# Optimization experiments

Measured on AMD Instinct MI355X. Metric: run time of the kernel, lower is better.

## Reference

```python
import jax, jax.numpy as jnp
import numpy as np

SCALING = 32.0 / 16  # alpha / rank


def setup_inputs() -> dict:
    key = jax.random.key(0)
    k1, k2, k3, k4, k5 = jax.random.split(key, 5)
    B, S, IN, OUT, R = 4, 2048, 4096, 4096, 16
    x = jax.random.normal(k1, (B, S, IN), dtype=jnp.float32)
    weight = jax.random.normal(k2, (OUT, IN), dtype=jnp.float32) * 0.02
    lora_a_w = jax.random.normal(k3, (R, IN), dtype=jnp.float32) * 0.02
    lora_b_w = jax.random.normal(k4, (OUT, R), dtype=jnp.float32) * 0.02
    magnitude = jax.random.uniform(k5, (OUT,), dtype=jnp.float32) + 0.5
    return {"x": x, "weight": weight, "lora_a_w": lora_a_w,
            "lora_b_w": lora_b_w, "magnitude": magnitude}


def reference(x, weight, lora_a_w, lora_b_w, magnitude):
    # base linear: x @ W^T  -> [..., out_dim]
    base_out = jnp.einsum('bsi,oi->bso', x, weight)
    # low-rank path (dropout is identity at p=0.0)
    lora_out = jnp.einsum('bsr,or->bso', jnp.einsum('bsi,ri->bsr', x, lora_a_w), lora_b_w)
    # merged low-rank weight B @ A (torch uses an eye-matrix trick; direct matmul is equivalent)
    lora_weight = lora_b_w @ lora_a_w  # [out, in]
    # row-wise norm of adapted weight; detached in the original
    weight_norm = jax.lax.stop_gradient(
        jnp.linalg.norm(weight + SCALING * lora_weight, axis=1))  # [out]
    mag_norm_scale = (magnitude / weight_norm)[None, None, :]  # [1,1,out]
    dora_out = (mag_norm_scale - 1.0) * base_out + mag_norm_scale * lora_out * SCALING
    return dora_out + base_out
```

## Files before the change

### kernel.cpp

```cpp
#include <hip/hip_runtime.h>
#include <hip/hip_bf16.h>
#include <stdint.h>

#define M_DIM 8192
#define N_DIM 4096
#define K_DIM 4096
#define R_DIM 16

#define PREP_BLOCKS 256
#define CAST_BLOCKS 8192

typedef __attribute__((ext_vector_type(8))) short bf16x8;
typedef __attribute__((ext_vector_type(4))) float f32x4;

__device__ __forceinline__ unsigned short f2bf(float f) {
  union { float f; unsigned int u; } v; v.f = f;
  unsigned int r = 0x7FFFu + ((v.u >> 16) & 1u);
  return (unsigned short)((v.u + r) >> 16);
}

__device__ __forceinline__ void gload16(const unsigned short* g, unsigned short* l) {
  __builtin_amdgcn_global_load_lds(
      (const __attribute__((address_space(1))) void*)g,
      (__attribute__((address_space(3))) void*)l,
      16, 0, 0);
}

__global__ void __launch_bounds__(256) prep_kernel(
    const float4* __restrict__ x4, ushort4* __restrict__ xbf4,
    const float* __restrict__ W, const float* __restrict__ Aw,
    const float* __restrict__ Bw, const float* __restrict__ mag,
    unsigned short* __restrict__ wbf, float* __restrict__ scale) {
  const int tid = threadIdx.x;

  if (blockIdx.x >= PREP_BLOCKS) {
    const int base = (blockIdx.x - PREP_BLOCKS) * 1024 + tid;
    #pragma unroll
    for (int u = 0; u < 4; ++u) {
      const int i = base + u * 256;
      float4 f = x4[i];
      ushort4 o;
      o.x = f2bf(f.x); o.y = f2bf(f.y); o.z = f2bf(f.z); o.w = f2bf(f.w);
      xbf4[i] = o;
    }
    return;
  }

  __shared__ float AwS[16 * 1024];
  __shared__ float BoS[16 * 16];
  __shared__ float red[16 * 4];
  const int o0 = blockIdx.x * 16;

  BoS[tid] = Bw[(o0 + (tid >> 4)) * R_DIM + (tid & 15)];

  float ss[16];
  #pragma unroll
  for (int i = 0; i < 16; ++i) ss[i] = 0.f;

  const float4* W4  = (const float4*)W;
  const float4* Aw4 = (const float4*)Aw;
  ushort4* wbf4 = (ushort4*)wbf;

  for (int c = 0; c < 4; ++c) {
    __syncthreads();
    #pragma unroll
    for (int t = tid; t < 4096; t += 256) {
      const int r  = t >> 8;
      const int j4 = t & 255;
      ((float4*)AwS)[r * 256 + j4] = Aw4[(size_t)r * 1024 + c * 256 + j4];
    }
    __syncthreads();
    #pragma unroll 4
    for (int i = 0; i < 16; ++i) {
      float4 w = W4[((size_t)(o0 + i) * K_DIM + c * 1024) / 4 + tid];
      float4 acc = {0.f, 0.f, 0.f, 0.f};
      #pragma unroll
      for (int r = 0; r < R_DIM; ++r) {
        const float b = BoS[i * 16 + r];
        const float4 a = ((const float4*)AwS)[r * 256 + tid];
        acc.x += b * a.x; acc.y += b * a.y; acc.z += b * a.z; acc.w += b * a.w;
      }
      float4 v;
      v.x = w.x + 2.f * acc.x; v.y = w.y + 2.f * acc.y;
      v.z = w.z + 2.f * acc.z; v.w = w.w + 2.f * acc.w;
      ss[i] += v.x * v.x + v.y * v.y + v.z * v.z + v.w * v.w;
      ushort4 o;
      o.x = f2bf(v.x); o.y = f2bf(v.y); o.z = f2bf(v.z); o.w = f2bf(v.w);
      wbf4[((size_t)(o0 + i) * K_DIM + c * 1024) / 4 + tid] = o;
    }
  }

  const int lane = tid & 63, wave = tid >> 6;
  #pragma unroll
  for (int i = 0; i < 16; ++i) {
    float s = ss[i];
    #pragma unroll
    for (int off = 32; off > 0; off >>= 1) s += __shfl_down(s, off, 64);
    if (lane == 0) red[i * 4 + wave] = s;
  }
  __syncthreads();
  if (tid < 16) {
    const float s = red[tid * 4] + red[tid * 4 + 1] + red[tid * 4 + 2] + red[tid * 4 + 3];
    scale[o0 + tid] = mag[o0 + tid] / sqrtf(s);
  }
}

__global__ void __launch_bounds__(256)
dora_gemm(const unsigned short* __restrict__ A,
          const unsigned short* __restrict__ Bt,
          const float* __restrict__ scale,
          float* __restrict__ C) {
  __shared__ __align__(16) unsigned short As[128 * 32];
  __shared__ __align__(16) unsigned short Bs[128 * 32];
  const int tid  = threadIdx.x;
  const int lane = tid & 63;
  const int wave = tid >> 6;
  const int bM = blockIdx.y * 128;
  const int bN = blockIdx.x * 128;

  const int sr = lane >> 2;
  const int sc = (((lane & 3) ^ ((lane >> 3) & 3)) * 8);
  const unsigned short* pa0 = A  + (size_t)(bM + wave * 32 + sr) * K_DIM + sc;
  const unsigned short* pa1 = pa0 + (size_t)16 * K_DIM;
  const unsigned short* pb0 = Bt + (size_t)(bN + wave * 32 + sr) * K_DIM + sc;
  const unsigned short* pb1 = pb0 + (size_t)16 * K_DIM;
  unsigned short* lA0 = &As[wave * 32 * 32];
  unsigned short* lA1 = lA0 + 16 * 32;
  unsigned short* lB0 = &Bs[wave * 32 * 32];
  unsigned short* lB1 = lB0 + 16 * 32;

  const int fr = lane & 15;
  const int fq = lane >> 4;
  const int xr = (fr >> 1) & 3;
  const int cA = (fq ^ xr) * 8;
  const int wM = (wave >> 1) * 64;
  const int wN = (wave & 1) * 64;

  f32x4 acc[4][4];
  #pragma unroll
  for (int i = 0; i < 4; ++i)
    #pragma unroll
    for (int j = 0; j < 4; ++j) acc[i][j] = (f32x4){0.f, 0.f, 0.f, 0.f};

  for (int k0 = 0; k0 < K_DIM; k0 += 32) {
    gload16(pa0 + k0, lA0);
    gload16(pa1 + k0, lA1);
    gload16(pb0 + k0, lB0);
    gload16(pb1 + k0, lB1);
    __syncthreads();
    bf16x8 aF[4], bF[4];
    #pragma unroll
    for (int mt = 0; mt < 4; ++mt)
      aF[mt] = *(const bf16x8*)&As[(wM + mt * 16 + fr) * 32 + cA];
    #pragma unroll
    for (int nt = 0; nt < 4; ++nt)
      bF[nt] = *(const bf16x8*)&Bs[(wN + nt * 16 + fr) * 32 + cA];
    #pragma unroll
    for (int mt = 0; mt < 4; ++mt)
      #pragma unroll
      for (int nt = 0; nt < 4; ++nt)
        acc[mt][nt] = __builtin_amdgcn_mfma_f32_16x16x32_bf16(aF[mt], bF[nt], acc[mt][nt], 0, 0, 0);
    __syncthreads();
  }

  float scv[4];
  #pragma unroll
  for (int nt = 0; nt < 4; ++nt) scv[nt] = scale[bN + wN + nt * 16 + fr];
  #pragma unroll
  for (int mt = 0; mt < 4; ++mt) {
    const int m0 = bM + wM + mt * 16 + fq * 4;
    #pragma unroll
    for (int nt = 0; nt < 4; ++nt) {
      const int n = bN + wN + nt * 16 + fr;
      #pragma unroll
      for (int r = 0; r < 4; ++r)
        C[(size_t)(m0 + r) * N_DIM + n] = acc[mt][nt][r] * scv[nt];
    }
  }
}

extern "C" void kernel_launch(void* const* d_in, const int* in_sizes, int n_in,
                              void* d_out, int out_size, void* d_ws, size_t ws_size,
                              hipStream_t stream) {
  const float* x   = (const float*)d_in[0];
  const float* W   = (const float*)d_in[1];
  const float* la  = (const float*)d_in[2];
  const float* lb  = (const float*)d_in[3];
  const float* mag = (const float*)d_in[4];
  float* out = (float*)d_out;

  unsigned short* xbf = (unsigned short*)d_ws;
  unsigned short* wbf = (unsigned short*)((char*)d_ws + (size_t)M_DIM * K_DIM * 2);
  float* scale = (float*)((char*)d_ws + (size_t)M_DIM * K_DIM * 2 + (size_t)N_DIM * K_DIM * 2);

  prep_kernel<<<PREP_BLOCKS + CAST_BLOCKS, 256, 0, stream>>>(
      (const float4*)x, (ushort4*)xbf, W, la, lb, mag, wbf, scale);
  dim3 grid(N_DIM / 128, M_DIM / 128);
  dora_gemm<<<grid, 256, 0, stream>>>(xbf, wbf, scale, out);
}
```

Before: 595.2 us.

## Double GEMM K-tile to 64 with 8-way XOR swizzle, restructure prep kernel

The GEMM now stages a 64-wide K slice per iteration instead of 32, using an 8-column XOR swizzle and two MFMA sub-steps per tile. This halves the number of barrier pairs and loop iterations. The prep kernel shrinks its shared A-weight buffer from 64KB to 16KB by processing 16 chunks of 256 columns, giving each wave 4 output rows. The x cast blocks each handle twice as many elements. The larger GEMM LDS tile raises shared memory per block, while the smaller prep footprint should improve occupancy there.

Result: slower. 619.7 us (+4.1%).

```diff
diff --git a/kernel.cpp b/kernel.cpp
--- a/kernel.cpp
+++ b/kernel.cpp
@@ -8,7 +8,7 @@
 #define R_DIM 16
 
 #define PREP_BLOCKS 256
-#define CAST_BLOCKS 8192
+#define CAST_BLOCKS 4096
 
 typedef __attribute__((ext_vector_type(8))) short bf16x8;
 typedef __attribute__((ext_vector_type(4))) float f32x4;
@@ -28,15 +28,15 @@
 
 __global__ void __launch_bounds__(256) prep_kernel(
     const float4* __restrict__ x4, ushort4* __restrict__ xbf4,
-    const float* __restrict__ W, const float* __restrict__ Aw,
+    const float4* __restrict__ W4, const float4* __restrict__ Aw4,
     const float* __restrict__ Bw, const float* __restrict__ mag,
-    unsigned short* __restrict__ wbf, float* __restrict__ scale) {
+    ushort4* __restrict__ wbf4, float* __restrict__ scale) {
   const int tid = threadIdx.x;
 
   if (blockIdx.x >= PREP_BLOCKS) {
-    const int base = (blockIdx.x - PREP_BLOCKS) * 1024 + tid;
+    const int base = (blockIdx.x - PREP_BLOCKS) * 2048 + tid;
     #pragma unroll
-    for (int u = 0; u < 4; ++u) {
+    for (int u = 0; u < 8; ++u) {
       const int i = base + u * 256;
       float4 f = x4[i];
       ushort4 o;
@@ -46,63 +46,53 @@
     return;
   }
 
-  __shared__ float AwS[16 * 1024];
+  __shared__ float4 AwS[16 * 64];
   __shared__ float BoS[16 * 16];
-  __shared__ float red[16 * 4];
+  __shared__ float red[16];
   const int o0 = blockIdx.x * 16;
+  const int g  = tid >> 6;
+  const int j  = tid & 63;
 
   BoS[tid] = Bw[(o0 + (tid >> 4)) * R_DIM + (tid & 15)];
 
-  float ss[16];
-  #pragma unroll
-  for (int i = 0; i < 16; ++i) ss[i] = 0.f;
+  float ss[4] = {0.f, 0.f, 0.f, 0.f};
 
-  const float4* W4  = (const float4*)W;
-  const float4* Aw4 = (const float4*)Aw;
-  ushort4* wbf4 = (ushort4*)wbf;
-
-  for (int c = 0; c < 4; ++c) {
+  for (int c = 0; c < 16; ++c) {
     __syncthreads();
     #pragma unroll
-    for (int t = tid; t < 4096; t += 256) {
-      const int r  = t >> 8;
-      const int j4 = t & 255;
-      ((float4*)AwS)[r * 256 + j4] = Aw4[(size_t)r * 1024 + c * 256 + j4];
-    }
+    for (int f = tid; f < 1024; f += 256)
+      AwS[f] = Aw4[(size_t)(f >> 6) * 1024 + c * 64 + (f & 63)];
     __syncthreads();
-    #pragma unroll 4
-    for (int i = 0; i < 16; ++i) {
-      float4 w = W4[((size_t)(o0 + i) * K_DIM + c * 1024) / 4 + tid];
+    #pragma unroll
+    for (int ii = 0; ii < 4; ++ii) {
+      const int i = g * 4 + ii;
+      float4 w = W4[(size_t)(o0 + i) * 1024 + c * 64 + j];
       float4 acc = {0.f, 0.f, 0.f, 0.f};
       #pragma unroll
       for (int r = 0; r < R_DIM; ++r) {
         const float b = BoS[i * 16 + r];
-        const float4 a = ((const float4*)AwS)[r * 256 + tid];
+        const float4 a = AwS[r * 64 + j];
         acc.x += b * a.x; acc.y += b * a.y; acc.z += b * a.z; acc.w += b * a.w;
       }
       float4 v;
       v.x = w.x + 2.f * acc.x; v.y = w.y + 2.f * acc.y;
       v.z = w.z + 2.f * acc.z; v.w = w.w + 2.f * acc.w;
-      ss[i] += v.x * v.x + v.y * v.y + v.z * v.z + v.w * v.w;
+      ss[ii] += v.x * v.x + v.y * v.y + v.z * v.z + v.w * v.w;
       ushort4 o;
       o.x = f2bf(v.x); o.y = f2bf(v.y); o.z = f2bf(v.z); o.w = f2bf(v.w);
-      wbf4[((size_t)(o0 + i) * K_DIM + c * 1024) / 4 + tid] = o;
+      wbf4[(size_t)(o0 + i) * 1024 + c * 64 + j] = o;
     }
   }
 
-  const int lane = tid & 63, wave = tid >> 6;
   #pragma unroll
-  for (int i = 0; i < 16; ++i) {
-    float s = ss[i];
+  for (int ii = 0; ii < 4; ++ii) {
+    float s = ss[ii];
     #pragma unroll
     for (int off = 32; off > 0; off >>= 1) s += __shfl_down(s, off, 64);
-    if (lane == 0) red[i * 4 + wave] = s;
+    if (j == 0) red[g * 4 + ii] = s;
   }
   __syncthreads();
-  if (tid < 16) {
-    const float s = red[tid * 4] + red[tid * 4 + 1] + red[tid * 4 + 2] + red[tid * 4 + 3];
-    scale[o0 + tid] = mag[o0 + tid] / sqrtf(s);
-  }
+  if (tid < 16) scale[o0 + tid] = mag[o0 + tid] / sqrtf(red[tid]);
 }
 
 __global__ void __launch_bounds__(256)
@@ -110,29 +100,23 @@
           const unsigned short* __restrict__ Bt,
           const float* __restrict__ scale,
           float* __restrict__ C) {
-  __shared__ __align__(16) unsigned short As[128 * 32];
-  __shared__ __align__(16) unsigned short Bs[128 * 32];
+  __shared__ __align__(16) unsigned short As[128 * 64];
+  __shared__ __align__(16) unsigned short Bs[128 * 64];
   const int tid  = threadIdx.x;
   const int lane = tid & 63;
   const int wave = tid >> 6;
   const int bM = blockIdx.y * 128;
   const int bN = blockIdx.x * 128;
 
-  const int sr = lane >> 2;
-  const int sc = (((lane & 3) ^ ((lane >> 3) & 3)) * 8);
-  const unsigned short* pa0 = A  + (size_t)(bM + wave * 32 + sr) * K_DIM + sc;
-  const unsigned short* pa1 = pa0 + (size_t)16 * K_DIM;
-  const unsigned short* pb0 = Bt + (size_t)(bN + wave * 32 + sr) * K_DIM + sc;
-  const unsigned short* pb1 = pb0 + (size_t)16 * K_DIM;
-  unsigned short* lA0 = &As[wave * 32 * 32];
-  unsigned short* lA1 = lA0 + 16 * 32;
-  unsigned short* lB0 = &Bs[wave * 32 * 32];
-  unsigned short* lB1 = lB0 + 16 * 32;
+  const int sr = lane >> 3;
+  const int sc = (((lane & 7) ^ sr) * 8);
+  const unsigned short* pa = A  + (size_t)(bM + wave * 32 + sr) * K_DIM + sc;
+  const unsigned short* pb = Bt + (size_t)(bN + wave * 32 + sr) * K_DIM + sc;
+  unsigned short* lA = &As[wave * 32 * 64];
+  unsigned short* lB = &Bs[wave * 32 * 64];
 
   const int fr = lane & 15;
   const int fq = lane >> 4;
-  const int xr = (fr >> 1) & 3;
-  const int cA = (fq ^ xr) * 8;
   const int wM = (wave >> 1) * 64;
   const int wN = (wave & 1) * 64;
 
@@ -140,26 +124,30 @@
   #pragma unroll
   for (int i = 0; i < 4; ++i)
     #pragma unroll
-    for (int j = 0; j < 4; ++j) acc[i][j] = (f32x4){0.f, 0.f, 0.f, 0.f};
+    for (int jj = 0; jj < 4; ++jj) acc[i][jj] = (f32x4){0.f, 0.f, 0.f, 0.f};
 
-  for (int k0 = 0; k0 < K_DIM; k0 += 32) {
-    gload16(pa0 + k0, lA0);
-    gload16(pa1 + k0, lA1);
-    gload16(pb0 + k0, lB0);
-    gload16(pb1 + k0, lB1);
+  for (int k0 = 0; k0 < K_DIM; k0 += 64) {
+    #pragma unroll
+    for (int jj = 0; jj < 4; ++jj) {
+      gload16(pa + (size_t)jj * 8 * K_DIM + k0, lA + jj * 512);
+      gload16(pb + (size_t)jj * 8 * K_DIM + k0, lB + jj * 512);
+    }
     __syncthreads();
-    bf16x8 aF[4], bF[4];
     #pragma unroll
-    for (int mt = 0; mt < 4; ++mt)
-      aF[mt] = *(const bf16x8*)&As[(wM + mt * 16 + fr) * 32 + cA];
-    #pragma unroll
-    for (int nt = 0; nt < 4; ++nt)
-      bF[nt] = *(const bf16x8*)&Bs[(wN + nt * 16 + fr) * 32 + cA];
-    #pragma unroll
-    for (int mt = 0; mt < 4; ++mt)
+    for (int h = 0; h < 2; ++h) {
+      bf16x8 aF[4], bF[4];
+      #pragma unroll
+      for (int mt = 0; mt < 4; ++mt)
+        aF[mt] = *(const bf16x8*)&As[(wM + mt * 16 + fr) * 64 + (((h * 4 + fq) ^ (fr & 7)) * 8)];
       #pragma unroll
       for (int nt = 0; nt < 4; ++nt)
-        acc[mt][nt] = __builtin_amdgcn_mfma_f32_16x16x32_bf16(aF[mt], bF[nt], acc[mt][nt], 0, 0, 0);
+        bF[nt] = *(const bf16x8*)&Bs[(wN + nt * 16 + fr) * 64 + (((h * 4 + fq) ^ (fr & 7)) * 8)];
+      #pragma unroll
+      for (int mt = 0; mt < 4; ++mt)
+        #pragma unroll
+        for (int nt = 0; nt < 4; ++nt)
+          acc[mt][nt] = __builtin_amdgcn_mfma_f32_16x16x32_bf16(aF[mt], bF[nt], acc[mt][nt], 0, 0, 0);
+    }
     __syncthreads();
   }
 
@@ -194,7 +182,8 @@
   float* scale = (float*)((char*)d_ws + (size_t)M_DIM * K_DIM * 2 + (size_t)N_DIM * K_DIM * 2);
 
   prep_kernel<<<PREP_BLOCKS + CAST_BLOCKS, 256, 0, stream>>>(
-      (const float4*)x, (ushort4*)xbf, W, la, lb, mag, wbf, scale);
+      (const float4*)x, (ushort4*)xbf, (const float4*)W, (const float4*)la,
+      lb, mag, (ushort4*)wbf, scale);
   dim3 grid(N_DIM / 128, M_DIM / 128);
   dora_gemm<<<grid, 256, 0, stream>>>(xbf, wbf, scale, out);
 }
```
